# Kernel optimization log

Hardware: AMD Instinct MI355X
Metric: run time of the kernel (lower is better)

## Reference

```python
import jax, jax.numpy as jnp
import numpy as np

N = 100000      # nodes
E = 600000      # directed edges (before self-loops)
NFEAT = 128
NHID = 128
NCLASS = 64


def setup_inputs() -> dict:
    key = jax.random.key(0)
    k1, k2, k3, k4 = jax.random.split(key, 4)
    x = jax.random.normal(k1, (N, NFEAT), dtype=jnp.float32)
    edge_index = jax.random.randint(k2, (2, E), 0, N, dtype=jnp.int32)
    # GCNConv learned params (Glorot-ish init), bias zeros as in PyG default
    W1 = jax.random.normal(k3, (NFEAT, NHID), dtype=jnp.float32) / jnp.sqrt(NFEAT)
    b1 = jnp.zeros((NHID,), dtype=jnp.float32)
    W2 = jax.random.normal(k4, (NHID, NCLASS), dtype=jnp.float32) / jnp.sqrt(NHID)
    b2 = jnp.zeros((NCLASS,), dtype=jnp.float32)
    return {"x": x, "edge_index": edge_index, "W1": W1, "b1": b1, "W2": W2, "b2": b2}


def _gcn_layer(x, src, dst, norm, W, b, n):
    # PyG GCNConv: linear transform, then normalized neighbor aggregation, then bias
    h = x @ W                                   # [N, out]
    msg = h[src] * norm[:, None]                # [E+N, out] gather + scale
    agg = jax.ops.segment_sum(msg, dst, num_segments=n)  # scatter-add
    return agg + b


def reference(x, edge_index, W1, b1, W2, b2):
    n = x.shape[0]
    # add self-loops (PyG gcn_norm default add_self_loops=True)
    loops = jnp.arange(n, dtype=edge_index.dtype)
    src = jnp.concatenate([edge_index[0], loops])
    dst = jnp.concatenate([edge_index[1], loops])
    # symmetric normalization: D^-1/2 (A+I) D^-1/2
    deg = jax.ops.segment_sum(jnp.ones_like(dst, dtype=x.dtype), dst, num_segments=n)
    d_inv_sqrt = jnp.where(deg > 0, jax.lax.rsqrt(deg), 0.0)
    norm = d_inv_sqrt[src] * d_inv_sqrt[dst]
    h = jax.nn.relu(_gcn_layer(x, src, dst, norm, W1, b1, n))
    # F.dropout with training=False is identity -> omitted in eval reference
    return _gcn_layer(h, src, dst, norm, W2, b2, n)
```

## Files before the change

### kernel.cpp

```cpp
#include <hip/hip_runtime.h>


typedef unsigned short u16;
typedef unsigned int u32;
typedef __attribute__((ext_vector_type(8))) short bf16x8;
typedef __attribute__((ext_vector_type(4))) float f32x4;

#define BSH 11
#define SEG 2560

__device__ __forceinline__ float b2f(u16 s) {
  return __uint_as_float(((u32)s) << 16);
}
__device__ __forceinline__ u16 f2b(float f) {
  u32 u = __float_as_uint(f);
  u32 r = (u + 0x7FFFu + ((u >> 16) & 1u)) >> 16;
  return (u16)r;
}
__device__ __forceinline__ u32 pk2(float a, float b) {
  return (u32)f2b(a) | ((u32)f2b(b) << 16);
}
__device__ __forceinline__ void dec8(uint4 v, float f[8]) {
  f[0] = __uint_as_float(v.x << 16);
  f[1] = __uint_as_float(v.x & 0xFFFF0000u);
  f[2] = __uint_as_float(v.y << 16);
  f[3] = __uint_as_float(v.y & 0xFFFF0000u);
  f[4] = __uint_as_float(v.z << 16);
  f[5] = __uint_as_float(v.z & 0xFFFF0000u);
  f[6] = __uint_as_float(v.w << 16);
  f[7] = __uint_as_float(v.w & 0xFFFF0000u);
}
__device__ __forceinline__ void fma8(uint4 v, float d, float acc[8]) {
  acc[0] = fmaf(__uint_as_float(v.x << 16), d, acc[0]);
  acc[1] = fmaf(__uint_as_float(v.x & 0xFFFF0000u), d, acc[1]);
  acc[2] = fmaf(__uint_as_float(v.y << 16), d, acc[2]);
  acc[3] = fmaf(__uint_as_float(v.y & 0xFFFF0000u), d, acc[3]);
  acc[4] = fmaf(__uint_as_float(v.z << 16), d, acc[4]);
  acc[5] = fmaf(__uint_as_float(v.z & 0xFFFF0000u), d, acc[5]);
  acc[6] = fmaf(__uint_as_float(v.w << 16), d, acc[6]);
  acc[7] = fmaf(__uint_as_float(v.w & 0xFFFF0000u), d, acc[7]);
}


__global__ __launch_bounds__(256) void prepcount_k(const void* __restrict__ W1,
                                                   const void* __restrict__ b1,
                                                   const void* __restrict__ W2,
                                                   const void* __restrict__ b2,
                                                   u16* __restrict__ W1b, u16* __restrict__ ob1,
                                                   u16* __restrict__ W2t, u16* __restrict__ ob2,
                                                   int* __restrict__ mode,
                                                   const int* __restrict__ dst,
                                                   int* __restrict__ cnt, int E, int NB) {
  __shared__ int cnt_s;
  const int tid = threadIdx.x;

  if ((int)blockIdx.x >= NB) {
    int e = ((int)blockIdx.x - NB) * 256 + tid;
    if (e < E) atomicAdd(&cnt[dst[e]], 1);
    return;
  }

  if (tid == 0) cnt_s = 0;
  __syncthreads();
  int c = 0;
  for (int j = tid; j < 4096; j += 256) {
    u32 e = (((const u16*)W1)[j] >> 7) & 0xFFu;
    if (e >= 100u && e <= 130u) c++;
  }
  atomicAdd(&cnt_s, c);
  __syncthreads();
  const int m = (cnt_s < 3328) ? 1 : 0;
  if (blockIdx.x == 0 && tid == 0) *mode = m;

  int i = blockIdx.x * 256 + tid;
  if (i < 24768) {
    int j = i;
    const void* src;
    u16* dstp;
    int sidx, didx;
    if (j < 16384) {
      src = W1; dstp = W1b; sidx = j; didx = j;
    } else if ((j -= 16384) < 128) {
      src = b1; dstp = ob1; sidx = j; didx = j;
    } else if ((j -= 128) < 8192) {
      int nn = j >> 7, k = j & 127;
      src = W2; dstp = W2t; sidx = k * 64 + nn; didx = j;
    } else {
      j -= 8192;
      src = b2; dstp = ob2; sidx = j; didx = j;
    }
    dstp[didx] = m ? f2b(((const float*)src)[sidx]) : ((const u16*)src)[sidx];
  }
}


__global__ __launch_bounds__(256) void scan1(const int* __restrict__ cnt,
                                             int* __restrict__ offs,
                                             int* __restrict__ bsum, int np) {
  __shared__ int lds[256];
  int t = threadIdx.x;
  int i = blockIdx.x * 256 + t;
  int v = cnt[i];
  lds[t] = v;
  __syncthreads();
#pragma unroll
  for (int off = 1; off < 256; off <<= 1) {
    int add = (t >= off) ? lds[t - off] : 0;
    __syncthreads();
    lds[t] += add;
    __syncthreads();
  }
  offs[i] = lds[t] - v;
  if (t == 0) bsum[blockIdx.x] = lds[255];
}

__global__ __launch_bounds__(256) void scan23(const int* __restrict__ offs,
                                              const int* __restrict__ bsum,
                                              int* __restrict__ cursor,
                                              const int* __restrict__ cnt,
                                              float* __restrict__ dinv,
                                              int4* __restrict__ ninfo,
                                              int* __restrict__ bstart,
                                              int* __restrict__ bcursor, int np) {
  __shared__ int lds[256];
  const int t = threadIdx.x, b = blockIdx.x;
  int part = 0;
  for (int k = t; k < b; k += 256) part += bsum[k];
  lds[t] = part;
  __syncthreads();
#pragma unroll
  for (int off = 128; off > 0; off >>= 1) {
    if (t < off) lds[t] += lds[t + off];
    __syncthreads();
  }
  const int pre = lds[0];
  int i = b * 256 + t;
  int o = offs[i] + pre;
  cursor[i] = o;
  if ((i & ((1 << BSH) - 1)) == 0) {
    bstart[i >> BSH] = o;
    bcursor[i >> BSH] = o;
  }
  int c = cnt[i];
  float dv = rsqrtf((float)c + 1.0f);
  dinv[i] = dv;
  ninfo[i] = make_int4(o, c, __float_as_int(dv), 0);
}


__global__ __launch_bounds__(256) void part_k(const int* __restrict__ src,
                                              const int* __restrict__ dst,
                                              int* __restrict__ bcursor,
                                              int2* __restrict__ tmp,
                                              int E, int NBK) {
  __shared__ int ls[SEG];
  __shared__ int ld_[SEG];
  __shared__ int hist[64];
  __shared__ int base_[64];
  const int tid = threadIdx.x;
  const int e0 = blockIdx.x * SEG;
  const int len = min(SEG, E - e0);

  if (tid < 64) hist[tid] = 0;
  __syncthreads();
  for (int j = tid; j < len; j += 256) {
    int s = src[e0 + j];
    int d = dst[e0 + j];
    ls[j] = s;
    ld_[j] = d;
    atomicAdd(&hist[d >> BSH], 1);
  }
  __syncthreads();
  if (tid < NBK) {
    int hh = hist[tid];
    base_[tid] = hh ? atomicAdd(&bcursor[tid], hh) : 0;
    hist[tid] = 0;
  }
  __syncthreads();
  for (int j = tid; j < len; j += 256) {
    int d = ld_[j];
    int bk = d >> BSH;
    int r = atomicAdd(&hist[bk], 1);
    tmp[base_[bk] + r] = make_int2(ls[j], d);
  }
}


__global__ __launch_bounds__(256) void scatter_k(const int2* __restrict__ tmp,
                                                 const int* __restrict__ bstart,
                                                 int* __restrict__ cursor,
                                                 const float* __restrict__ dinv,
                                                 int2* __restrict__ sp,
                                                 int E, int NBK) {
  const int x = blockIdx.x & 7;
  const int q = blockIdx.x >> 3;
  const int g = q >> 3, k = q & 7;
  const int b = x + (g << 3);
  if (b >= NBK) return;
  const int bs = bstart[b];
  const int be = (b + 1 < NBK) ? bstart[b + 1] : E;
  const int len = be - bs;
  const int s0 = bs + (int)(((long long)len * k) >> 3);
  const int s1 = bs + (int)(((long long)len * (k + 1)) >> 3);
  for (int e = s0 + threadIdx.x; e < s1; e += 256) {
    int2 p = tmp[e];
    float ds = dinv[p.x];
    int pos = atomicAdd(&cursor[p.y], 1);
    sp[pos] = make_int2(p.x, __float_as_int(ds));
  }
}


__global__ __launch_bounds__(256) void gemm1_k(const void* __restrict__ Araw,
                                               const u16* __restrict__ W,
                                               u16* __restrict__ out, int M,
                                               const int* __restrict__ mode) {
  __shared__ __align__(16) u16 Wt[128 * 136];
  __shared__ __align__(16) u16 As[64 * 136];
  const int tid = threadIdx.x;
  const int mcv = *mode;

  for (int idx = tid; idx < 128 * 128; idx += 256) {
    int n = idx & 127;
    int k = idx >> 7;
    Wt[n * 136 + k] = W[k * 128 + n];
  }
  __syncthreads();

  const int wv = tid >> 6, lane = tid & 63, lr = lane & 15, lq = lane >> 4;
  const int ntiles = (M + 63) >> 6;

  for (int t = blockIdx.x; t < ntiles; t += gridDim.x) {
    const int r0 = t * 64;
    __syncthreads();
    for (int idx = tid; idx < 64 * 16; idx += 256) {
      int row = idx >> 4, c = idx & 15;
      uint4 v = make_uint4(0u, 0u, 0u, 0u);
      if (r0 + row < M) {
        if (mcv) {
          const float* xf = (const float*)Araw + (size_t)(r0 + row) * 128 + c * 8;
          float4 f0 = *(const float4*)xf;
          float4 f1 = *(const float4*)(xf + 4);
          v.x = pk2(f0.x, f0.y);
          v.y = pk2(f0.z, f0.w);
          v.z = pk2(f1.x, f1.y);
          v.w = pk2(f1.z, f1.w);
        } else {
          v = *(const uint4*)((const u16*)Araw + (size_t)(r0 + row) * 128 + c * 8);
        }
      }
      *(uint4*)&As[row * 136 + c * 8] = v;
    }
    __syncthreads();

    bf16x8 a[4];
#pragma unroll
    for (int s = 0; s < 4; ++s)
      a[s] = *(const bf16x8*)&As[(wv * 16 + lr) * 136 + s * 32 + lq * 8];

#pragma unroll
    for (int nt = 0; nt < 8; ++nt) {
      f32x4 acc = {0.f, 0.f, 0.f, 0.f};
#pragma unroll
      for (int s = 0; s < 4; ++s) {
        bf16x8 b = *(const bf16x8*)&Wt[(nt * 16 + lr) * 136 + s * 32 + lq * 8];
        acc = __builtin_amdgcn_mfma_f32_16x16x32_bf16(a[s], b, acc, 0, 0, 0);
      }
#pragma unroll
      for (int r = 0; r < 4; ++r) {
        int row = r0 + wv * 16 + lq * 4 + r;
        if (row < M) out[(size_t)row * 128 + nt * 16 + lr] = f2b(acc[r]);
      }
    }
  }
}


__global__ __launch_bounds__(256) void fusedB_k(const u16* __restrict__ h,
                                                const int2* __restrict__ sp,
                                                const int4* __restrict__ ninfo,
                                                const u16* __restrict__ b1,
                                                const u16* __restrict__ W2t,
                                                u16* __restrict__ g, int n) {
  __shared__ __align__(16) u16 As[16 * 136];
  const int tid = threadIdx.x, wv = tid >> 6, lane = tid & 63;
  const int lq = lane >> 4, lr = lane & 15;
  const int base = blockIdx.x * 16;
  const int i = base + wv * 4 + lq;
  const bool valid = (i < n);

  int start = 0, c = 0;
  float di = 0.f;
  if (valid) {
    int4 ni = ninfo[i];
    start = ni.x;
    c = ni.y;
    di = __int_as_float(ni.z);
  }
  float acc[8];
  {
    uint4 v = valid ? *(const uint4*)(h + (size_t)i * 128 + lr * 8)
                    : make_uint4(0u, 0u, 0u, 0u);
    float f[8];
    dec8(v, f);
#pragma unroll
    for (int j = 0; j < 8; ++j) acc[j] = f[j] * di;
  }
  const int bl = lq * 16;
  for (int bs = 0; __any(bs < c); bs += 16) {
    int m = c - bs;
    m = m < 0 ? 0 : (m > 16 ? 16 : m);
    int s = 0, db = 0;
    if (lr < m) {
      int2 p = sp[start + bs + lr];
      s = p.x;
      db = p.y;
    }
    int mmw = m;
    mmw = max(mmw, __shfl_xor(mmw, 16));
    mmw = max(mmw, __shfl_xor(mmw, 32));
    for (int e = 0; e < mmw; e += 4) {
      int s0 = __shfl(s, bl + e), s1 = __shfl(s, bl + e + 1);
      int s2 = __shfl(s, bl + e + 2), s3 = __shfl(s, bl + e + 3);
      float d0 = __int_as_float(__shfl(db, bl + e));
      float d1 = __int_as_float(__shfl(db, bl + e + 1));
      float d2 = __int_as_float(__shfl(db, bl + e + 2));
      float d3 = __int_as_float(__shfl(db, bl + e + 3));
      uint4 v0 = *(const uint4*)(h + (size_t)s0 * 128 + lr * 8);
      uint4 v1 = *(const uint4*)(h + (size_t)s1 * 128 + lr * 8);
      uint4 v2 = *(const uint4*)(h + (size_t)s2 * 128 + lr * 8);
      uint4 v3 = *(const uint4*)(h + (size_t)s3 * 128 + lr * 8);
      fma8(v0, d0, acc);
      fma8(v1, d1, acc);
      fma8(v2, d2, acc);
      fma8(v3, d3, acc);
    }
  }
  {
    uint4 bv = *(const uint4*)(b1 + lr * 8);
    float bf[8];
    dec8(bv, bf);
    float o[8];
#pragma unroll
    for (int j = 0; j < 8; ++j) o[j] = fmaxf(fmaf(acc[j], di, bf[j]), 0.f);
    uint4 ov;
    ov.x = pk2(o[0], o[1]);
    ov.y = pk2(o[2], o[3]);
    ov.z = pk2(o[4], o[5]);
    ov.w = pk2(o[6], o[7]);
    *(uint4*)&As[(wv * 4 + lq) * 136 + lr * 8] = ov;
  }
  __syncthreads();

  bf16x8 a[4];
#pragma unroll
  for (int s = 0; s < 4; ++s)
    a[s] = *(const bf16x8*)&As[lr * 136 + s * 32 + lq * 8];
  {
    const int nt = wv;
    f32x4 acc4 = {0.f, 0.f, 0.f, 0.f};
#pragma unroll
    for (int s = 0; s < 4; ++s) {
      bf16x8 b = *(const bf16x8*)&W2t[(nt * 16 + lr) * 128 + s * 32 + lq * 8];
      acc4 = __builtin_amdgcn_mfma_f32_16x16x32_bf16(a[s], b, acc4, 0, 0, 0);
    }
#pragma unroll
    for (int r = 0; r < 4; ++r) {
      int row = base + lq * 4 + r;
      if (row < n) g[(size_t)row * 64 + nt * 16 + lr] = f2b(acc4[r]);
    }
  }
}


__global__ __launch_bounds__(256) void agg2_k(const u16* __restrict__ g,
                                              const int2* __restrict__ sp,
                                              const int4* __restrict__ ninfo,
                                              const u16* __restrict__ b2,
                                              void* __restrict__ outv, int n,
                                              const int* __restrict__ mode) {
  const int lane = threadIdx.x & 63;
  const int o8 = lane >> 3, l8 = lane & 7;
  const int i = blockIdx.x * 32 + (threadIdx.x >> 6) * 8 + o8;
  const bool valid = (i < n);

  int start = 0, c = 0;
  float di = 0.f;
  if (valid) {
    int4 ni = ninfo[i];
    start = ni.x;
    c = ni.y;
    di = __int_as_float(ni.z);
  }
  float acc[8];
  {
    uint4 v = valid ? *(const uint4*)(g + (size_t)i * 64 + l8 * 8)
                    : make_uint4(0u, 0u, 0u, 0u);
    float f[8];
    dec8(v, f);
#pragma unroll
    for (int j = 0; j < 8; ++j) acc[j] = f[j] * di;
  }
  const int bl = o8 * 8;
  for (int base = 0; __any(base < c); base += 8) {
    int m = c - base;
    m = m < 0 ? 0 : (m > 8 ? 8 : m);
    int s = 0, db = 0;
    if (l8 < m) {
      int2 p = sp[start + base + l8];
      s = p.x;
      db = p.y;
    }
    int mmw = m;
    mmw = max(mmw, __shfl_xor(mmw, 8));
    mmw = max(mmw, __shfl_xor(mmw, 16));
    mmw = max(mmw, __shfl_xor(mmw, 32));
    for (int e = 0; e < mmw; e += 4) {
      int s0 = __shfl(s, bl + e), s1 = __shfl(s, bl + e + 1);
      int s2 = __shfl(s, bl + e + 2), s3 = __shfl(s, bl + e + 3);
      float d0 = __int_as_float(__shfl(db, bl + e));
      float d1 = __int_as_float(__shfl(db, bl + e + 1));
      float d2 = __int_as_float(__shfl(db, bl + e + 2));
      float d3 = __int_as_float(__shfl(db, bl + e + 3));
      uint4 v0 = *(const uint4*)(g + (size_t)s0 * 64 + l8 * 8);
      uint4 v1 = *(const uint4*)(g + (size_t)s1 * 64 + l8 * 8);
      uint4 v2 = *(const uint4*)(g + (size_t)s2 * 64 + l8 * 8);
      uint4 v3 = *(const uint4*)(g + (size_t)s3 * 64 + l8 * 8);
      fma8(v0, d0, acc);
      fma8(v1, d1, acc);
      fma8(v2, d2, acc);
      fma8(v3, d3, acc);
    }
  }
  if (valid) {
    uint4 bv = *(const uint4*)(b2 + l8 * 8);
    float bf[8];
    dec8(bv, bf);
    float o[8];
#pragma unroll
    for (int j = 0; j < 8; ++j) o[j] = fmaf(acc[j], di, bf[j]);
    if (*mode) {
      float* op = (float*)outv + (size_t)i * 64 + l8 * 8;
      *(float4*)op = make_float4(o[0], o[1], o[2], o[3]);
      *(float4*)(op + 4) = make_float4(o[4], o[5], o[6], o[7]);
    } else {
      uint4 ov;
      ov.x = pk2(o[0], o[1]);
      ov.y = pk2(o[2], o[3]);
      ov.z = pk2(o[4], o[5]);
      ov.w = pk2(o[6], o[7]);
      *(uint4*)((u16*)outv + (size_t)i * 64 + l8 * 8) = ov;
    }
  }
}


extern "C" void kernel_launch(void* const* d_in, const int* in_sizes, int n_in,
                              void* d_out, int out_size, void* d_ws, size_t ws_size,
                              hipStream_t stream) {
  const void* x_raw  = d_in[0];
  const int*  ei     = (const int*)d_in[1];
  const void* W1_raw = d_in[2];
  const void* b1_raw = d_in[3];
  const void* W2_raw = d_in[4];
  const void* b2_raw = d_in[5];

  const int N = in_sizes[0] / 128;
  const int E = in_sizes[1] / 2;
  const int NP = ((N + 255) / 256) * 256;
  const int NB = NP / 256;
  const int NBK = (NP + (1 << BSH) - 1) >> BSH;
  const int NBG = (NBK + 7) >> 3;

  char* ws = (char*)d_ws;
  size_t off = 0;
  auto alloc = [&](size_t bytes) -> void* {
    void* p = ws + off;
    off = (off + bytes + 255) & ~(size_t)255;
    return p;
  };
  int*   mode    = (int*)alloc(4);
  int*   cnt     = (int*)alloc((size_t)NP * 4);
  float* dinv    = (float*)alloc((size_t)NP * 4);
  int*   offs    = (int*)alloc((size_t)NP * 4);
  int*   cursor  = (int*)alloc((size_t)NP * 4);
  int*   bsum    = (int*)alloc(1024 * 4);
  int*   bstart  = (int*)alloc(256 * 4);
  int*   bcursor = (int*)alloc(256 * 4);
  int4*  ninfo   = (int4*)alloc((size_t)NP * 16);
  int2*  sp      = (int2*)alloc((size_t)E * 8);
  int2*  tmp     = (int2*)alloc((size_t)E * 8);
  u16*   W1b     = (u16*)alloc((size_t)128 * 128 * 2);
  u16*   b1b     = (u16*)alloc(128 * 2);
  u16*   W2t     = (u16*)alloc((size_t)64 * 128 * 2);
  u16*   b2b     = (u16*)alloc(64 * 2);
  u16*   h       = (u16*)alloc((size_t)N * 128 * 2);
  u16*   g       = (u16*)alloc((size_t)N * 64 * 2);

  const int eb = (E + 255) / 256;
  const int pb = (E + SEG - 1) / SEG;

  hipMemsetAsync(cnt, 0, (size_t)NP * 4, stream);
  prepcount_k<<<NB + eb, 256, 0, stream>>>(W1_raw, b1_raw, W2_raw, b2_raw,
                                           W1b, b1b, W2t, b2b, mode,
                                           ei + E, cnt, E, NB);
  scan1<<<NB, 256, 0, stream>>>(cnt, offs, bsum, NP);
  scan23<<<NB, 256, 0, stream>>>(offs, bsum, cursor, cnt, dinv, ninfo,
                                 bstart, bcursor, NP);
  part_k<<<pb, 256, 0, stream>>>(ei, ei + E, bcursor, tmp, E, NBK);
  scatter_k<<<64 * NBG, 256, 0, stream>>>(tmp, bstart, cursor, dinv, sp, E, NBK);
  gemm1_k<<<512, 256, 0, stream>>>(x_raw, W1b, h, N, mode);
  fusedB_k<<<(N + 15) / 16, 256, 0, stream>>>(h, sp, ninfo, b1b, W2t, g, N);
  agg2_k<<<(N + 31) / 32, 256, 0, stream>>>(g, sp, ninfo, b2b, d_out, N, mode);
}
```

Baseline: 234.8 us.

## Rebuild CSR via bucket histogram and per-bucket LDS counting sort

```diff
diff --git a/kernel.cpp b/kernel.cpp
--- a/kernel.cpp
+++ b/kernel.cpp
@@ -6,12 +6,12 @@
 typedef __attribute__((ext_vector_type(8))) short bf16x8;
 typedef __attribute__((ext_vector_type(4))) float f32x4;
 
-#define BSH 11
+#define BSH 9
+#define BMSK ((1 << BSH) - 1)
+#define MAXBK 256
 #define SEG 2560
-
-__device__ __forceinline__ float b2f(u16 s) {
-  return __uint_as_float(((u32)s) << 16);
-}
+#define HISTB 128
+
 __device__ __forceinline__ u16 f2b(float f) {
   u32 u = __float_as_uint(f);
   u32 r = (u + 0x7FFFu + ((u >> 16) & 1u)) >> 16;
@@ -42,7 +42,7 @@
 }
 
 
-__global__ __launch_bounds__(256) void prepcount_k(const void* __restrict__ W1,
+__global__ __launch_bounds__(256) void prep_hist_k(const void* __restrict__ W1,
                                                    const void* __restrict__ b1,
                                                    const void* __restrict__ W2,
                                                    const void* __restrict__ b2,
@@ -50,16 +50,28 @@
                                                    u16* __restrict__ W2t, u16* __restrict__ ob2,
                                                    int* __restrict__ mode,
                                                    const int* __restrict__ dst,
-                                                   int* __restrict__ cnt, int E, int NB) {
+                                                   int* __restrict__ bhist,
+                                                   int E, int PREPB) {
+  const int tid = threadIdx.x;
+
+  if ((int)blockIdx.x >= PREPB) {
+    __shared__ int lh[MAXBK];
+    const int hb = (int)blockIdx.x - PREPB;
+    for (int j = tid; j < MAXBK; j += 256) lh[j] = 0;
+    __syncthreads();
+    const int chunk = (E + HISTB - 1) / HISTB;
+    const int e0 = hb * chunk;
+    const int e1 = min(E, e0 + chunk);
+    for (int e = e0 + tid; e < e1; e += 256) atomicAdd(&lh[dst[e] >> BSH], 1);
+    __syncthreads();
+    for (int j = tid; j < MAXBK; j += 256) {
+      int v = lh[j];
+      if (v) atomicAdd(&bhist[j], v);
+    }
+    return;
+  }
+
   __shared__ int cnt_s;
-  const int tid = threadIdx.x;
-
-  if ((int)blockIdx.x >= NB) {
-    int e = ((int)blockIdx.x - NB) * 256 + tid;
-    if (e < E) atomicAdd(&cnt[dst[e]], 1);
-    return;
-  }
-
   if (tid == 0) cnt_s = 0;
   __syncthreads();
   int c = 0;
@@ -94,119 +106,137 @@
 }
 
 
-__global__ __launch_bounds__(256) void scan1(const int* __restrict__ cnt,
-                                             int* __restrict__ offs,
-                                             int* __restrict__ bsum, int np) {
-  __shared__ int lds[256];
-  int t = threadIdx.x;
-  int i = blockIdx.x * 256 + t;
-  int v = cnt[i];
-  lds[t] = v;
-  __syncthreads();
-#pragma unroll
-  for (int off = 1; off < 256; off <<= 1) {
-    int add = (t >= off) ? lds[t - off] : 0;
-    __syncthreads();
-    lds[t] += add;
-    __syncthreads();
-  }
-  offs[i] = lds[t] - v;
-  if (t == 0) bsum[blockIdx.x] = lds[255];
-}
-
-__global__ __launch_bounds__(256) void scan23(const int* __restrict__ offs,
-                                              const int* __restrict__ bsum,
-                                              int* __restrict__ cursor,
-                                              const int* __restrict__ cnt,
-                                              float* __restrict__ dinv,
-                                              int4* __restrict__ ninfo,
-                                              int* __restrict__ bstart,
-                                              int* __restrict__ bcursor, int np) {
-  __shared__ int lds[256];
-  const int t = threadIdx.x, b = blockIdx.x;
-  int part = 0;
-  for (int k = t; k < b; k += 256) part += bsum[k];
-  lds[t] = part;
-  __syncthreads();
-#pragma unroll
-  for (int off = 128; off > 0; off >>= 1) {
-    if (t < off) lds[t] += lds[t + off];
-    __syncthreads();
-  }
-  const int pre = lds[0];
-  int i = b * 256 + t;
-  int o = offs[i] + pre;
-  cursor[i] = o;
-  if ((i & ((1 << BSH) - 1)) == 0) {
-    bstart[i >> BSH] = o;
-    bcursor[i >> BSH] = o;
-  }
-  int c = cnt[i];
-  float dv = rsqrtf((float)c + 1.0f);
-  dinv[i] = dv;
-  ninfo[i] = make_int4(o, c, __float_as_int(dv), 0);
-}
-
-
 __global__ __launch_bounds__(256) void part_k(const int* __restrict__ src,
                                               const int* __restrict__ dst,
-                                              int* __restrict__ bcursor,
+                                              const int* __restrict__ bhist,
+                                              int* __restrict__ boff,
                                               int2* __restrict__ tmp,
                                               int E, int NBK) {
   __shared__ int ls[SEG];
   __shared__ int ld_[SEG];
-  __shared__ int hist[64];
-  __shared__ int base_[64];
+  __shared__ int lh[MAXBK];
+  __shared__ int base_[MAXBK];
+  __shared__ int bsl[MAXBK];
   const int tid = threadIdx.x;
+
+  int ov = (tid < NBK) ? bhist[tid] : 0;
+  bsl[tid] = ov;
+  __syncthreads();
+#pragma unroll
+  for (int off = 1; off < 256; off <<= 1) {
+    int add = (tid >= off) ? bsl[tid - off] : 0;
+    __syncthreads();
+    bsl[tid] += add;
+    __syncthreads();
+  }
+  bsl[tid] -= ov;
+  if (tid < MAXBK) lh[tid] = 0;
+  __syncthreads();
+
   const int e0 = blockIdx.x * SEG;
   const int len = min(SEG, E - e0);
-
-  if (tid < 64) hist[tid] = 0;
-  __syncthreads();
   for (int j = tid; j < len; j += 256) {
     int s = src[e0 + j];
     int d = dst[e0 + j];
     ls[j] = s;
     ld_[j] = d;
-    atomicAdd(&hist[d >> BSH], 1);
+    atomicAdd(&lh[d >> BSH], 1);
   }
   __syncthreads();
   if (tid < NBK) {
-    int hh = hist[tid];
-    base_[tid] = hh ? atomicAdd(&bcursor[tid], hh) : 0;
-    hist[tid] = 0;
+    int hh = lh[tid];
+    base_[tid] = hh ? bsl[tid] + atomicAdd(&boff[tid], hh) : 0;
+    lh[tid] = 0;
   }
   __syncthreads();
   for (int j = tid; j < len; j += 256) {
     int d = ld_[j];
     int bk = d >> BSH;
-    int r = atomicAdd(&hist[bk], 1);
+    int r = atomicAdd(&lh[bk], 1);
     tmp[base_[bk] + r] = make_int2(ls[j], d);
   }
 }
 
 
-__global__ __launch_bounds__(256) void scatter_k(const int2* __restrict__ tmp,
-                                                 const int* __restrict__ bstart,
-                                                 int* __restrict__ cursor,
-                                                 const float* __restrict__ dinv,
-                                                 int2* __restrict__ sp,
-                                                 int E, int NBK) {
-  const int x = blockIdx.x & 7;
-  const int q = blockIdx.x >> 3;
-  const int g = q >> 3, k = q & 7;
-  const int b = x + (g << 3);
-  if (b >= NBK) return;
-  const int bs = bstart[b];
-  const int be = (b + 1 < NBK) ? bstart[b + 1] : E;
-  const int len = be - bs;
-  const int s0 = bs + (int)(((long long)len * k) >> 3);
-  const int s1 = bs + (int)(((long long)len * (k + 1)) >> 3);
-  for (int e = s0 + threadIdx.x; e < s1; e += 256) {
+__global__ __launch_bounds__(256) void nbuild_k(const int2* __restrict__ tmp,
+                                                const int* __restrict__ bhist,
+                                                float* __restrict__ dinv,
+                                                int4* __restrict__ ninfo,
+                                                int* __restrict__ spI,
+                                                int np, int NBK) {
+  __shared__ int bsl[MAXBK];
+  __shared__ int cntl[1 << BSH];
+  __shared__ int curl[1 << BSH];
+  __shared__ int sc2[256];
+  const int tid = threadIdx.x;
+  const int b = blockIdx.x;
+
+  int ov = (tid < NBK) ? bhist[tid] : 0;
+  bsl[tid] = ov;
+  __syncthreads();
+#pragma unroll
+  for (int off = 1; off < 256; off <<= 1) {
+    int add = (tid >= off) ? bsl[tid - off] : 0;
+    __syncthreads();
+    bsl[tid] += add;
+    __syncthreads();
+  }
+  bsl[tid] -= ov;
+  cntl[tid] = 0;
+  cntl[tid + 256] = 0;
+  curl[tid] = 0;
+  curl[tid + 256] = 0;
+  __syncthreads();
+
+  const int bs = bsl[b];
+  const int be = bs + bhist[b];
+  const int lo = b << BSH;
+
+  for (int e = bs + tid; e < be; e += 256) {
     int2 p = tmp[e];
-    float ds = dinv[p.x];
-    int pos = atomicAdd(&cursor[p.y], 1);
-    sp[pos] = make_int2(p.x, __float_as_int(ds));
+    atomicAdd(&cntl[p.y & BMSK], 1);
+  }
+  __syncthreads();
+
+  const int c0 = cntl[2 * tid];
+  const int c1 = cntl[2 * tid + 1];
+  const int s2 = c0 + c1;
+  sc2[tid] = s2;
+  __syncthreads();
+#pragma unroll
+  for (int off = 1; off < 256; off <<= 1) {
+    int add = (tid >= off) ? sc2[tid - off] : 0;
+    __syncthreads();
+    sc2[tid] += add;
+    __syncthreads();
+  }
+  const int excl = sc2[tid] - s2;
+  const int e0n = excl;
+  const int e1n = excl + c0;
+
+  {
+    int i0 = lo + 2 * tid;
+    if (i0 < np) {
+      float dv = rsqrtf((float)c0 + 1.0f);
+      dinv[i0] = dv;
+      ninfo[i0] = make_int4(bs + e0n, c0, __float_as_int(dv), 0);
+    }
+    int i1 = i0 + 1;
+    if (i1 < np) {
+      float dv = rsqrtf((float)c1 + 1.0f);
+      dinv[i1] = dv;
+      ninfo[i1] = make_int4(bs + e1n, c1, __float_as_int(dv), 0);
+    }
+  }
+  cntl[2 * tid] = e0n;
+  cntl[2 * tid + 1] = e1n;
+  __syncthreads();
+
+  for (int e = bs + tid; e < be; e += 256) {
+    int2 p = tmp[e];
+    int loc = p.y & BMSK;
+    int r = atomicAdd(&curl[loc], 1);
+    spI[bs + cntl[loc] + r] = p.x;
   }
 }
 
@@ -277,8 +307,9 @@
 
 
 __global__ __launch_bounds__(256) void fusedB_k(const u16* __restrict__ h,
-                                                const int2* __restrict__ sp,
+                                                const int* __restrict__ spI,
                                                 const int4* __restrict__ ninfo,
+                                                const float* __restrict__ dinv,
                                                 const u16* __restrict__ b1,
                                                 const u16* __restrict__ W2t,
                                                 u16* __restrict__ g, int n) {
@@ -310,11 +341,11 @@
   for (int bs = 0; __any(bs < c); bs += 16) {
     int m = c - bs;
     m = m < 0 ? 0 : (m > 16 ? 16 : m);
-    int s = 0, db = 0;
+    int s = 0;
+    float dv = 0.f;
     if (lr < m) {
-      int2 p = sp[start + bs + lr];
-      s = p.x;
-      db = p.y;
+      s = spI[start + bs + lr];
+      dv = dinv[s];
     }
     int mmw = m;
     mmw = max(mmw, __shfl_xor(mmw, 16));
@@ -322,10 +353,10 @@
     for (int e = 0; e < mmw; e += 4) {
       int s0 = __shfl(s, bl + e), s1 = __shfl(s, bl + e + 1);
       int s2 = __shfl(s, bl + e + 2), s3 = __shfl(s, bl + e + 3);
-      float d0 = __int_as_float(__shfl(db, bl + e));
-      float d1 = __int_as_float(__shfl(db, bl + e + 1));
-      float d2 = __int_as_float(__shfl(db, bl + e + 2));
-      float d3 = __int_as_float(__shfl(db, bl + e + 3));
+      float d0 = __shfl(dv, bl + e);
+      float d1 = __shfl(dv, bl + e + 1);
+      float d2 = __shfl(dv, bl + e + 2);
+      float d3 = __shfl(dv, bl + e + 3);
       uint4 v0 = *(const uint4*)(h + (size_t)s0 * 128 + lr * 8);
       uint4 v1 = *(const uint4*)(h + (size_t)s1 * 128 + lr * 8);
       uint4 v2 = *(const uint4*)(h + (size_t)s2 * 128 + lr * 8);
@@ -374,8 +405,9 @@
 
 
 __global__ __launch_bounds__(256) void agg2_k(const u16* __restrict__ g,
-                                              const int2* __restrict__ sp,
+                                              const int* __restrict__ spI,
                                               const int4* __restrict__ ninfo,
+                                              const float* __restrict__ dinv,
                                               const u16* __restrict__ b2,
                                               void* __restrict__ outv, int n,
                                               const int* __restrict__ mode) {
@@ -405,11 +437,11 @@
   for (int base = 0; __any(base < c); base += 8) {
     int m = c - base;
     m = m < 0 ? 0 : (m > 8 ? 8 : m);
-    int s = 0, db = 0;
+    int s = 0;
+    float dv = 0.f;
     if (l8 < m) {
-      int2 p = sp[start + base + l8];
-      s = p.x;
-      db = p.y;
+      s = spI[start + base + l8];
+      dv = dinv[s];
     }
     int mmw = m;
     mmw = max(mmw, __shfl_xor(mmw, 8));
@@ -418,10 +450,10 @@
     for (int e = 0; e < mmw; e += 4) {
       int s0 = __shfl(s, bl + e), s1 = __shfl(s, bl + e + 1);
       int s2 = __shfl(s, bl + e + 2), s3 = __shfl(s, bl + e + 3);
-      float d0 = __int_as_float(__shfl(db, bl + e));
-      float d1 = __int_as_float(__shfl(db, bl + e + 1));
-      float d2 = __int_as_float(__shfl(db, bl + e + 2));
-      float d3 = __int_as_float(__shfl(db, bl + e + 3));
+      float d0 = __shfl(dv, bl + e);
+      float d1 = __shfl(dv, bl + e + 1);
+      float d2 = __shfl(dv, bl + e + 2);
+      float d3 = __shfl(dv, bl + e + 3);
       uint4 v0 = *(const uint4*)(g + (size_t)s0 * 64 + l8 * 8);
       uint4 v1 = *(const uint4*)(g + (size_t)s1 * 64 + l8 * 8);
       uint4 v2 = *(const uint4*)(g + (size_t)s2 * 64 + l8 * 8);
@@ -468,9 +500,8 @@
   const int N = in_sizes[0] / 128;
   const int E = in_sizes[1] / 2;
   const int NP = ((N + 255) / 256) * 256;
-  const int NB = NP / 256;
   const int NBK = (NP + (1 << BSH) - 1) >> BSH;
-  const int NBG = (NBK + 7) >> 3;
+  const int PREPB = (24768 + 255) / 256;
 
   char* ws = (char*)d_ws;
   size_t off = 0;
@@ -480,15 +511,12 @@
     return p;
   };
   int*   mode    = (int*)alloc(4);
-  int*   cnt     = (int*)alloc((size_t)NP * 4);
+  int*   bz      = (int*)alloc((size_t)2 * MAXBK * 4);
+  int*   bhist   = bz;
+  int*   boff    = bz + MAXBK;
   float* dinv    = (float*)alloc((size_t)NP * 4);
-  int*   offs    = (int*)alloc((size_t)NP * 4);
-  int*   cursor  = (int*)alloc((size_t)NP * 4);
-  int*   bsum    = (int*)alloc(1024 * 4);
-  int*   bstart  = (int*)alloc(256 * 4);
-  int*   bcursor = (int*)alloc(256 * 4);
   int4*  ninfo   = (int4*)alloc((size_t)NP * 16);
-  int2*  sp      = (int2*)alloc((size_t)E * 8);
+  int*   spI     = (int*)alloc((size_t)E * 4);
   int2*  tmp     = (int2*)alloc((size_t)E * 8);
   u16*   W1b     = (u16*)alloc((size_t)128 * 128 * 2);
   u16*   b1b     = (u16*)alloc(128 * 2);
@@ -497,19 +525,15 @@
   u16*   h       = (u16*)alloc((size_t)N * 128 * 2);
   u16*   g       = (u16*)alloc((size_t)N * 64 * 2);
 
-  const int eb = (E + 255) / 256;
   const int pb = (E + SEG - 1) / SEG;
 
-  hipMemsetAsync(cnt, 0, (size_t)NP * 4, stream);
-  prepcount_k<<<NB + eb, 256, 0, stream>>>(W1_raw, b1_raw, W2_raw, b2_raw,
-                                           W1b, b1b, W2t, b2b, mode,
-                                           ei + E, cnt, E, NB);
-  scan1<<<NB, 256, 0, stream>>>(cnt, offs, bsum, NP);
-  scan23<<<NB, 256, 0, stream>>>(offs, bsum, cursor, cnt, dinv, ninfo,
-                                 bstart, bcursor, NP);
-  part_k<<<pb, 256, 0, stream>>>(ei, ei + E, bcursor, tmp, E, NBK);
-  scatter_k<<<64 * NBG, 256, 0, stream>>>(tmp, bstart, cursor, dinv, sp, E, NBK);
+  hipMemsetAsync(bz, 0, (size_t)2 * MAXBK * 4, stream);
+  prep_hist_k<<<PREPB + HISTB, 256, 0, stream>>>(W1_raw, b1_raw, W2_raw, b2_raw,
+                                                 W1b, b1b, W2t, b2b, mode,
+                                                 ei + E, bhist, E, PREPB);
+  part_k<<<pb, 256, 0, stream>>>(ei, ei + E, bhist, boff, tmp, E, NBK);
+  nbuild_k<<<NBK, 256, 0, stream>>>(tmp, bhist, dinv, ninfo, spI, NP, NBK);
   gemm1_k<<<512, 256, 0, stream>>>(x_raw, W1b, h, N, mode);
-  fusedB_k<<<(N + 15) / 16, 256, 0, stream>>>(h, sp, ninfo, b1b, W2t, g, N);
-  agg2_k<<<(N + 31) / 32, 256, 0, stream>>>(g, sp, ninfo, b2b, d_out, N, mode);
-}
+  fusedB_k<<<(N + 15) / 16, 256, 0, stream>>>(h, spI, ninfo, dinv, b1b, W2t, g, N);
+  agg2_k<<<(N + 31) / 32, 256, 0, stream>>>(g, spI, ninfo, dinv, b2b, d_out, N, mode);
+}
```

New measurement: 194.4 us. 17.2% less time.
